# Kernel tuning notes

Hardware: AMD Instinct MI355X
Metric: run time of the kernel (lower is better)

## Reference

```python
import jax, jax.numpy as jnp
import numpy as np

B, EMB, H, G, F, CH, O, OC, KT = 4096, 256, 256, 8, 96, 16, 5, 10, 5
BN_EPS = 1e-3


def _grouped_linear(x, w):
    # x: [B, I], w: [G, I//G, O//G] -> [B, O]
    b = x.shape[0]
    g, ig, og = w.shape
    xg = x.reshape(b, g, ig)
    return jnp.einsum('bgi,gio->bgo', xg, w).reshape(b, g * og)


def _gru_cell(x, h, k, rk, bias):
    # keras GRUCell, reset_after=True; gate order z, r, h; bias: [2, 3H]
    xs = x @ k + bias[0]
    hs = h @ rk + bias[1]
    xz, xr, xh = jnp.split(xs, 3, axis=-1)
    hz, hr, hh = jnp.split(hs, 3, axis=-1)
    z = jax.nn.sigmoid(xz + hz)
    r = jax.nn.sigmoid(xr + hr)
    cand = jnp.tanh(xh + r * hh)
    return z * h + (1.0 - z) * cand


def setup_inputs() -> dict:
    key = jax.random.key(0)
    ks = jax.random.split(key, 20)
    w = lambda i, shape: (jax.random.normal(ks[i], shape, dtype=jnp.float32) * 0.05)
    inp = {
        'emb': jax.random.normal(ks[0], (B, EMB), dtype=jnp.float32),
        'c0': jax.random.normal(ks[1], (B, 1, F, CH), dtype=jnp.float32),
        'df_dec_state': jax.random.normal(ks[2], (B, 2 * H), dtype=jnp.float32),
        'df_convp_buf': jax.random.normal(ks[3], (B, KT - 1, F, CH), dtype=jnp.float32),
        'w_in': w(4, (G, EMB // G, H // G)),
        'gru_k0': w(5, (H, 3 * H)),
        'gru_rk0': w(6, (H, 3 * H)),
        'gru_b0': w(7, (2, 3 * H)),
        'gru_k1': w(8, (H, 3 * H)),
        'gru_rk1': w(9, (H, 3 * H)),
        'gru_b1': w(10, (2, 3 * H)),
        'w_out': w(11, (G, H // G, (F * OC) // G)),
        'fc_a_w': w(12, (H, 1)),
        'fc_a_b': jnp.zeros((1,), dtype=jnp.float32),
        'conv_w': w(13, (KT, 1, CH // 2, OC)),  # grouped conv, groups=gcd(16,10)=2
        'pw_w': w(14, (OC, OC)),                # 1x1 pointwise, no bias
        'bn_gamma': jnp.ones((OC,), dtype=jnp.float32),
        'bn_beta': jnp.zeros((OC,), dtype=jnp.float32),
        'bn_mean': jnp.zeros((OC,), dtype=jnp.float32),
        'bn_var': jnp.ones((OC,), dtype=jnp.float32),
    }
    return inp


def reference(emb, c0, df_dec_state, df_convp_buf,
              w_in, gru_k0, gru_rk0, gru_b0, gru_k1, gru_rk1, gru_b1,
              w_out, fc_a_w, fc_a_b, conv_w, pw_w,
              bn_gamma, bn_beta, bn_mean, bn_var):
    b = emb.shape[0]
    # SqueezedGRUStep: grouped linear in-proj + ReLU
    x_in = jax.nn.relu(_grouped_linear(emb, w_in))  # [B, H]
    h0 = df_dec_state[:, :H]
    h1 = df_dec_state[:, H:]
    out0 = _gru_cell(x_in, h0, gru_k0, gru_rk0, gru_b0)
    out1 = _gru_cell(out0, h1, gru_k1, gru_rk1, gru_b1)
    new_state = jnp.concatenate([out0, out1], axis=-1)  # [B, 2H]
    c = out1 + x_in  # gru_skip = identity

    # causal conv step: concat buffer + current frame -> [B, KT, F, CH]
    x = jnp.concatenate([df_convp_buf, c0], axis=1)
    new_buf = x[:, 1:, :, :]
    # grouped conv (groups=2), kernel (KT,1), valid over the KT frames -> last frame
    xg = x.reshape(b, KT, F, 2, CH // 2)                 # [B,T,F,g,i]
    wg = conv_w.reshape(KT, CH // 2, 2, OC // 2)         # [T,i,g,o]
    y = jnp.einsum('btfgi,tigo->bfgo', xg, wg).reshape(b, F, OC)
    # separable pointwise 1x1 conv
    y = y @ pw_w
    # batch norm (inference) + relu
    inv = jax.lax.rsqrt(bn_var + BN_EPS)
    y = (y - bn_mean) * inv * bn_gamma + bn_beta
    c0_out = jax.nn.relu(y)                              # [B, F, OC]

    alpha = jax.nn.sigmoid(emb @ jnp.zeros_like(fc_a_w) + c @ fc_a_w + fc_a_b)  # [B,1]
    c_out = jnp.tanh(_grouped_linear(c, w_out)).reshape(b, F, OC)
    c_out = c_out + c0_out
    # DfOutputReshapeMF: [B,1,F,O*2] -> [B,O,1,F,2]
    coefs = c_out.reshape(b, 1, F, O, 2).transpose(0, 3, 1, 2, 4)
    return (coefs, alpha, new_state, new_buf)
```

## Files before the change

kernel.cpp:

```cpp
#include <hip/hip_runtime.h>

typedef unsigned short u16;
typedef __attribute__((ext_vector_type(8))) u16 u16x8;
typedef __attribute__((ext_vector_type(8))) __bf16 bf16x8;
typedef __attribute__((ext_vector_type(4))) float f32x4;

#define ALPHA_OFF   3932160
#define NST_OFF     3936256
#define NBUF_OFF    6033408

__device__ __forceinline__ u16 f2bf(float f) {
  unsigned u = __builtin_bit_cast(unsigned, f);
  u += 0x7fffu + ((u >> 16) & 1u);
  return (u16)(u >> 16);
}
__device__ __forceinline__ float bf2f(u16 v) {
  return __builtin_bit_cast(float, (unsigned)v << 16);
}
__device__ __forceinline__ float fsig(float x) { return 1.f / (1.f + __expf(-x)); }
__device__ __forceinline__ float ftanh(float x) {
  x = fminf(15.f, fmaxf(-15.f, x));
  float e = __expf(2.f * x);
  return (e - 1.f) / (e + 1.f);
}
__device__ __forceinline__ f32x4 mfma16(u16x8 a, u16x8 b, f32x4 c) {
  return __builtin_amdgcn_mfma_f32_16x16x32_bf16(
      __builtin_bit_cast(bf16x8, a), __builtin_bit_cast(bf16x8, b), c, 0, 0, 0);
}
__device__ __forceinline__ void gload16(const void* g, void* l) {
  __builtin_amdgcn_global_load_lds(
      (const __attribute__((address_space(1))) void*)g,
      (__attribute__((address_space(3))) void*)l, 16, 0, 0);
}

__global__ __launch_bounds__(256) void prep_all_kernel(
    const float* __restrict__ emb, const float* __restrict__ dec,
    const float* __restrict__ w_in,
    const float* __restrict__ gk0, const float* __restrict__ grk0,
    const float* __restrict__ gk1, const float* __restrict__ grk1,
    const float* __restrict__ w_out,
    u16* __restrict__ A0, u16* __restrict__ A1, u16* __restrict__ W2,
    u16* __restrict__ W3) {
  int bi = blockIdx.x, tid = threadIdx.x;
  if (bi < 192) {
    __shared__ u16 tl[64][65];
    int nb = bi % 12, kb = (bi / 12) % 8, L = bi / 96;
    const float* src = (kb < 4) ? (L ? gk1 : gk0) : (L ? grk1 : grk0);
    int kbase = (kb & 3) * 64;
    u16* dst = W2 + (size_t)L * 768 * 512;
    int c = tid & 63, r4 = tid >> 6;
    for (int rr = 0; rr < 64; rr += 4) {
      int k = kbase + rr + r4, n = nb * 64 + c;
      tl[rr + r4][c] = f2bf(src[(size_t)k * 768 + n]);
    }
    __syncthreads();
    for (int rr = 0; rr < 64; rr += 4) {
      int n = nb * 64 + rr + r4, k = kb * 64 + c;
      dst[(size_t)n * 512 + k] = tl[c][rr + r4];
    }
  } else if (bi < 200) {
    int g = bi - 192;
    for (int i = tid; i < 4096; i += 256) {
      int col = i >> 5, k = i & 31;
      float v = (col < 120) ? w_out[(size_t)g * 3840 + k * 120 + col] : 0.f;
      W3[(size_t)g * 4096 + i] = f2bf(v);
    }
  } else {
    __shared__ float el[4][256];
    int rowBase = (bi - 200) * 4;
    {
      int r = tid >> 6, c4 = tid & 63;
      *(float4*)&el[r][c4 * 4] = ((const float4*)emb)[(size_t)(rowBase + r) * 64 + c4];
    }
    int g = tid >> 5, o = tid & 31;
    float wr[32];
#pragma unroll
    for (int i = 0; i < 32; ++i) wr[i] = w_in[g * 1024 + i * 32 + o];
    __syncthreads();
#pragma unroll
    for (int r = 0; r < 4; ++r) {
      float acc = 0.f;
#pragma unroll
      for (int i = 0; i < 32; ++i) acc += el[r][g * 32 + i] * wr[i];
      A0[(size_t)(rowBase + r) * 512 + tid] = f2bf(fmaxf(acc, 0.f));
    }
    const float4* d4 = (const float4*)dec;
#pragma unroll
    for (int j = 0; j < 2; ++j) {
      int idx = tid + j * 256;
      int r = idx >> 7, c4 = idx & 127;
      float4 v = d4[(size_t)(rowBase + r) * 128 + c4];
      ushort4 q;
      q.x = f2bf(v.x); q.y = f2bf(v.y); q.z = f2bf(v.z); q.w = f2bf(v.w);
      u16* dst = (c4 < 64) ? A0 + (size_t)(rowBase + r) * 512 + 256 + c4 * 4
                           : A1 + (size_t)(rowBase + r) * 512 + 256 + (c4 - 64) * 4;
      *(ushort4*)dst = q;
    }
  }
}

template <int LAYER>
__global__ __launch_bounds__(256) void gru_kernel(
    const u16* __restrict__ Ain,
    const u16* __restrict__ W2,
    const float* __restrict__ dec,
    const float* __restrict__ bias,
    float* __restrict__ nst,
    u16* __restrict__ a1out,
    const u16* __restrict__ xbf,
    u16* __restrict__ c_bf) {
  __shared__ __align__(16) u16 lsA[2][32][32];
  __shared__ __align__(16) u16 lsB[2][3][64][32];
  int tid = threadIdx.x, lane = tid & 63, wave = tid >> 6;
  int m0 = lane & 15, quad = lane >> 4;
  int rowBase = blockIdx.x * 32, jz = blockIdx.y * 64, cw = wave * 16;
  f32x4 acc[4][2];
#pragma unroll
  for (int gi = 0; gi < 4; ++gi)
#pragma unroll
    for (int rb = 0; rb < 2; ++rb) acc[gi][rb] = (f32x4){0.f, 0.f, 0.f, 0.f};

  int rS = tid >> 2, qS = tid & 3;
  auto stage = [&](int buf, int k0) {
    if (tid < 128)
      gload16(Ain + (size_t)(rowBase + rS) * 512 + k0 + qS * 8,
              &lsA[buf][rS][qS * 8]);
#pragma unroll
    for (int g = 0; g < 3; ++g)
      gload16(W2 + (size_t)(g * 256 + jz + rS) * 512 + k0 + qS * 8,
              &lsB[buf][g][rS][qS * 8]);
  };

  stage(0, 0);
  for (int step = 0; step < 16; ++step) {
    __syncthreads();
    if (step < 15) stage((step & 1) ^ 1, (step + 1) * 32);
    int cur = step & 1;
    u16x8 av[2], bv[3];
#pragma unroll
    for (int rb = 0; rb < 2; ++rb)
      av[rb] = *(const u16x8*)&lsA[cur][rb * 16 + m0][quad * 8];
#pragma unroll
    for (int g = 0; g < 3; ++g)
      bv[g] = *(const u16x8*)&lsB[cur][g][cw + m0][quad * 8];
#pragma unroll
    for (int rb = 0; rb < 2; ++rb) {
      acc[0][rb] = mfma16(av[rb], bv[0], acc[0][rb]);
      acc[1][rb] = mfma16(av[rb], bv[1], acc[1][rb]);
    }
    if (step < 8) {
#pragma unroll
      for (int rb = 0; rb < 2; ++rb) acc[2][rb] = mfma16(av[rb], bv[2], acc[2][rb]);
    } else {
#pragma unroll
      for (int rb = 0; rb < 2; ++rb) acc[3][rb] = mfma16(av[rb], bv[2], acc[3][rb]);
    }
  }

  int col = jz + cw + m0;
  float bz = bias[col] + bias[768 + col];
  float br = bias[256 + col] + bias[1024 + col];
  float bxh = bias[512 + col];
  float bhh = bias[1280 + col];
  const int hoff = LAYER ? 256 : 0;
#pragma unroll
  for (int rb = 0; rb < 2; ++rb) {
#pragma unroll
    for (int i = 0; i < 4; ++i) {
      int row = rowBase + rb * 16 + quad * 4 + i;
      float h = dec[(size_t)row * 512 + hoff + col];
      float z = fsig(acc[0][rb][i] + bz);
      float r = fsig(acc[1][rb][i] + br);
      float cand = ftanh(acc[2][rb][i] + bxh + r * (acc[3][rb][i] + bhh));
      float o = z * h + (1.f - z) * cand;
      nst[(size_t)row * 512 + hoff + col] = o;
      if (LAYER == 0) {
        a1out[(size_t)row * 512 + col] = f2bf(o);
      } else {
        float c = o + bf2f(xbf[(size_t)row * 512 + col]);
        c_bf[(size_t)row * 256 + col] = f2bf(c);
      }
    }
  }
}

__global__ __launch_bounds__(256) void wout_kernel(
    const u16* __restrict__ c_bf, const u16* __restrict__ W3,
    float* __restrict__ outc) {
  __shared__ __align__(16) u16 lsA[64][32];
  __shared__ __align__(16) u16 lsB[128][32];
  int tid = threadIdx.x, lane = tid & 63, wave = tid >> 6;
  int m0 = lane & 15, quad = lane >> 4;
  int rowBase = blockIdx.x * 64, g = blockIdx.y;
  {
    int r = tid >> 2, q = tid & 3;
    gload16(c_bf + (size_t)(rowBase + r) * 256 + g * 32 + q * 8, &lsA[r][q * 8]);
    gload16(W3 + (size_t)g * 4096 + (size_t)r * 32 + q * 8, &lsB[r][q * 8]);
    gload16(W3 + (size_t)g * 4096 + (size_t)(64 + r) * 32 + q * 8, &lsB[64 + r][q * 8]);
  }
  __syncthreads();
  int cw = wave * 32;
  f32x4 acc[4][2];
#pragma unroll
  for (int rb = 0; rb < 4; ++rb)
#pragma unroll
    for (int cb = 0; cb < 2; ++cb) acc[rb][cb] = (f32x4){0.f, 0.f, 0.f, 0.f};
  u16x8 bv[2];
#pragma unroll
  for (int cb = 0; cb < 2; ++cb)
    bv[cb] = *(const u16x8*)&lsB[cw + cb * 16 + m0][quad * 8];
#pragma unroll
  for (int rb = 0; rb < 4; ++rb) {
    u16x8 av = *(const u16x8*)&lsA[rb * 16 + m0][quad * 8];
#pragma unroll
    for (int cb = 0; cb < 2; ++cb) acc[rb][cb] = mfma16(av, bv[cb], acc[rb][cb]);
  }
#pragma unroll
  for (int cb = 0; cb < 2; ++cb) {
    int cg = cw + cb * 16 + m0;
    if (cg < 120) {
      int e0 = g * 120 + cg;
      int ff = e0 / 10, p = e0 % 10;
      int fin = (p >> 1) * 192 + ff * 2 + (p & 1);
#pragma unroll
      for (int rb = 0; rb < 4; ++rb)
#pragma unroll
        for (int i = 0; i < 4; ++i)
          outc[(size_t)(rowBase + rb * 16 + quad * 4 + i) * 960 + fin] =
              ftanh(acc[rb][cb][i]);
    }
  }
}

__global__ __launch_bounds__(384) void head_kernel(
    const float* __restrict__ convp, const float* __restrict__ c0,
    const u16* __restrict__ c_bf,
    const float* __restrict__ conv_w, const float* __restrict__ pw_w,
    const float* __restrict__ bng, const float* __restrict__ bnb,
    const float* __restrict__ bnm, const float* __restrict__ bnv,
    const float* __restrict__ fca_w, const float* __restrict__ fca_b,
    float* __restrict__ outp) {
  __shared__ __align__(16) float cw2[640];
  __shared__ float pws[100];
  __shared__ float bsc[10], bsh[10];
  __shared__ float ybuf[2][96][11];
  __shared__ float ared[6];
  int tid = threadIdx.x, lane = tid & 63, wave = tid >> 6;
  int row = tid >= 192, t = tid - row * 192;
  int brow = blockIdx.x * 2 + row;
  int f = t >> 1, half = t & 1;
  const float4* cp4 = (const float4*)convp;
  const float4* c04 = (const float4*)c0;
  float4* nb4 = (float4*)(outp + NBUF_OFF);

  size_t sbase = (size_t)brow * 1536 + f * 4 + half * 2;
  size_t cbase = (size_t)brow * 384 + f * 4 + half * 2;
  float4 xa0 = cp4[sbase];         float4 xb0 = cp4[sbase + 1];
  float4 xa1 = cp4[sbase + 384];   float4 xb1 = cp4[sbase + 385];
  float4 xa2 = cp4[sbase + 768];   float4 xb2 = cp4[sbase + 769];
  float4 xa3 = cp4[sbase + 1152];  float4 xb3 = cp4[sbase + 1153];
  float4 xa4 = c04[cbase];         float4 xb4 = c04[cbase + 1];
  float tmp[5];
#pragma unroll
  for (int k = 0; k < 5; ++k)
    tmp[k] = outp[(size_t)brow * 960 + t + k * 192];
  float ap = bf2f(c_bf[(size_t)brow * 256 + t]) * fca_w[t];
  if (t < 64) ap += bf2f(c_bf[(size_t)brow * 256 + 192 + t]) * fca_w[192 + t];

  for (int i = tid; i < 400; i += 384) {
    int tt = i / 80, rr = (i % 80) / 10, h = (i % 10) / 5, j = i % 5;
    cw2[((tt * 8 + rr) * 2 + h) * 8 + j] = conv_w[i];
  }
  if (tid < 100) pws[tid] = pw_w[tid];
  if (tid < 10) {
    float s = bng[tid] * rsqrtf(bnv[tid] + 1e-3f);
    bsc[tid] = s;
    bsh[tid] = bnb[tid] - bnm[tid] * s;
  }
  nb4[sbase] = xa1;         nb4[sbase + 1] = xb1;
  nb4[sbase + 384] = xa2;   nb4[sbase + 385] = xb2;
  nb4[sbase + 768] = xa3;   nb4[sbase + 769] = xb3;
  nb4[sbase + 1152] = xa4;  nb4[sbase + 1153] = xb4;
#pragma unroll
  for (int off = 32; off > 0; off >>= 1) ap += __shfl_down(ap, off, 64);
  if (lane == 0) ared[wave] = ap;
  __syncthreads();
  float a5[5] = {0.f, 0.f, 0.f, 0.f, 0.f};
#define CI(XF, T, I)                                                        \
  {                                                                         \
    const float* wp = &cw2[(((T) * 8 + (I)) * 2 + half) * 8];               \
    float4 w03 = *(const float4*)wp;                                        \
    float w4 = wp[4];                                                       \
    a5[0] += (XF) * w03.x; a5[1] += (XF) * w03.y; a5[2] += (XF) * w03.z;    \
    a5[3] += (XF) * w03.w; a5[4] += (XF) * w4;                              \
  }
#define CTAP(VA, VB, T)                                                     \
  CI(VA.x, T, 0) CI(VA.y, T, 1) CI(VA.z, T, 2) CI(VA.w, T, 3)               \
  CI(VB.x, T, 4) CI(VB.y, T, 5) CI(VB.z, T, 6) CI(VB.w, T, 7)
  CTAP(xa0, xb0, 0)
  CTAP(xa1, xb1, 1)
  CTAP(xa2, xb2, 2)
  CTAP(xa3, xb3, 3)
  CTAP(xa4, xb4, 4)
#undef CTAP
#undef CI
#pragma unroll
  for (int j = 0; j < 5; ++j) ybuf[row][f][half * 5 + j] = a5[j];
  __syncthreads();
  if (t == 0)
    outp[ALPHA_OFF + brow] =
        fsig(ared[row * 3] + ared[row * 3 + 1] + ared[row * 3 + 2] + fca_b[0]);
  float vals[5];
#pragma unroll
  for (int k = 0; k < 5; ++k) {
    int p = k * 2 + half;
    float y2 = 0.f;
#pragma unroll
    for (int j = 0; j < 10; ++j) y2 += ybuf[row][f][j] * pws[j * 10 + p];
    vals[k] = fmaxf(y2 * bsc[p] + bsh[p], 0.f) + tmp[k];
  }
#pragma unroll
  for (int k = 0; k < 5; ++k)
    outp[(size_t)brow * 960 + t + k * 192] = vals[k];
}

extern "C" void kernel_launch(void* const* d_in, const int* in_sizes, int n_in,
                              void* d_out, int out_size, void* d_ws, size_t ws_size,
                              hipStream_t stream) {
  const float* emb    = (const float*)d_in[0];
  const float* c0     = (const float*)d_in[1];
  const float* dec    = (const float*)d_in[2];
  const float* convp  = (const float*)d_in[3];
  const float* w_in   = (const float*)d_in[4];
  const float* gk0    = (const float*)d_in[5];
  const float* grk0   = (const float*)d_in[6];
  const float* gb0    = (const float*)d_in[7];
  const float* gk1    = (const float*)d_in[8];
  const float* grk1   = (const float*)d_in[9];
  const float* gb1    = (const float*)d_in[10];
  const float* w_out  = (const float*)d_in[11];
  const float* fca_w  = (const float*)d_in[12];
  const float* fca_b  = (const float*)d_in[13];
  const float* conv_w = (const float*)d_in[14];
  const float* pw_w   = (const float*)d_in[15];
  const float* bng    = (const float*)d_in[16];
  const float* bnb    = (const float*)d_in[17];
  const float* bnm    = (const float*)d_in[18];
  const float* bnv    = (const float*)d_in[19];
  float* out = (float*)d_out;
  char* ws = (char*)d_ws;
  u16* A0   = (u16*)(ws + 0);
  u16* A1   = (u16*)(ws + 4194304);
  u16* c_bf = (u16*)(ws + 8388608);
  u16* W2   = (u16*)(ws + 10485760);
  u16* W3   = (u16*)(ws + 12058624);

  prep_all_kernel<<<dim3(1224), 256, 0, stream>>>(emb, dec, w_in,
                                                  gk0, grk0, gk1, grk1, w_out,
                                                  A0, A1, W2, W3);
  gru_kernel<0><<<dim3(128, 4), 256, 0, stream>>>(A0, W2, dec, gb0,
                                                  out + NST_OFF, A1, nullptr, nullptr);
  gru_kernel<1><<<dim3(128, 4), 256, 0, stream>>>(A1, W2 + 768 * 512, dec, gb1,
                                                  out + NST_OFF, nullptr, A0, c_bf);
  wout_kernel<<<dim3(64, 8), 256, 0, stream>>>(c_bf, W3, out);
  head_kernel<<<dim3(2048), 384, 0, stream>>>(convp, c0, c_bf, conv_w, pw_w,
                                              bng, bnb, bnm, bnv, fca_w, fca_b, out);
}
```

Before: 307.0 us.

## Fold conv head into GRU layer-0 launch and alpha into wout kernel

Removes the separate head kernel. Its causal conv, pointwise, BN and buffer-shift work now runs in extra blocks appended to the layer-0 GRU grid, one batch row per block, which lets it overlap with the GEMM blocks. The alpha dot product moves into the g==0 blocks of the wout kernel, and wout now adds tanh output onto the conv result already in the output buffer. This drops one launch and the head's second pass over the output, at the cost of a read-modify-write in wout and 64 idle lanes in each conv block.

Result: no change. 308.8 us (+0.6%).

```diff
diff --git a/kernel.cpp b/kernel.cpp
--- a/kernel.cpp
+++ b/kernel.cpp
@@ -108,12 +108,98 @@
     float* __restrict__ nst,
     u16* __restrict__ a1out,
     const u16* __restrict__ xbf,
-    u16* __restrict__ c_bf) {
-  __shared__ __align__(16) u16 lsA[2][32][32];
-  __shared__ __align__(16) u16 lsB[2][3][64][32];
-  int tid = threadIdx.x, lane = tid & 63, wave = tid >> 6;
+    u16* __restrict__ c_bf,
+    const float* __restrict__ convp, const float* __restrict__ c0f,
+    const float* __restrict__ conv_w, const float* __restrict__ pw_w,
+    const float* __restrict__ bng, const float* __restrict__ bnb,
+    const float* __restrict__ bnm, const float* __restrict__ bnv,
+    float* __restrict__ outp) {
+  __shared__ __align__(16) char smem[28672];
+  int bi = blockIdx.x, tid = threadIdx.x;
+
+  if (LAYER == 0 && bi >= 512) {
+    int b = bi - 512;
+    float* cw2 = (float*)smem;
+    float* pws = (float*)(smem + 2560);
+    float* bscp = (float*)(smem + 2960);
+    float* bshp = (float*)(smem + 3000);
+    float (*ybuf)[11] = (float (*)[11])(smem + 3040);
+    int t = tid, f = t >> 1, half = t & 1;
+    bool act = t < 192;
+    const float4* cp4 = (const float4*)convp;
+    const float4* c04 = (const float4*)c0f;
+    float4* nb4 = (float4*)(outp + NBUF_OFF);
+    size_t sbase = (size_t)b * 1536 + f * 4 + half * 2;
+    size_t cbase = (size_t)b * 384 + f * 4 + half * 2;
+    float4 xa0 = {0,0,0,0}, xb0 = {0,0,0,0}, xa1 = {0,0,0,0}, xb1 = {0,0,0,0};
+    float4 xa2 = {0,0,0,0}, xb2 = {0,0,0,0}, xa3 = {0,0,0,0}, xb3 = {0,0,0,0};
+    float4 xa4 = {0,0,0,0}, xb4 = {0,0,0,0};
+    if (act) {
+      xa0 = cp4[sbase];         xb0 = cp4[sbase + 1];
+      xa1 = cp4[sbase + 384];   xb1 = cp4[sbase + 385];
+      xa2 = cp4[sbase + 768];   xb2 = cp4[sbase + 769];
+      xa3 = cp4[sbase + 1152];  xb3 = cp4[sbase + 1153];
+      xa4 = c04[cbase];         xb4 = c04[cbase + 1];
+    }
+    for (int i = tid; i < 400; i += 256) {
+      int tt = i / 80, rr = (i % 80) / 10, h = (i % 10) / 5, j = i % 5;
+      cw2[((tt * 8 + rr) * 2 + h) * 8 + j] = conv_w[i];
+    }
+    if (tid < 100) pws[tid] = pw_w[tid];
+    if (tid < 10) {
+      float s = bng[tid] * rsqrtf(bnv[tid] + 1e-3f);
+      bscp[tid] = s;
+      bshp[tid] = bnb[tid] - bnm[tid] * s;
+    }
+    if (act) {
+      nb4[sbase] = xa1;         nb4[sbase + 1] = xb1;
+      nb4[sbase + 384] = xa2;   nb4[sbase + 385] = xb2;
+      nb4[sbase + 768] = xa3;   nb4[sbase + 769] = xb3;
+      nb4[sbase + 1152] = xa4;  nb4[sbase + 1153] = xb4;
+    }
+    __syncthreads();
+    if (act) {
+      float a5[5] = {0.f, 0.f, 0.f, 0.f, 0.f};
+#define CI(XF, T, I)                                                        \
+  {                                                                         \
+    const float* wp = &cw2[(((T) * 8 + (I)) * 2 + half) * 8];               \
+    float4 w03 = *(const float4*)wp;                                        \
+    float w4 = wp[4];                                                       \
+    a5[0] += (XF) * w03.x; a5[1] += (XF) * w03.y; a5[2] += (XF) * w03.z;    \
+    a5[3] += (XF) * w03.w; a5[4] += (XF) * w4;                              \
+  }
+#define CTAP(VA, VB, T)                                                     \
+  CI(VA.x, T, 0) CI(VA.y, T, 1) CI(VA.z, T, 2) CI(VA.w, T, 3)               \
+  CI(VB.x, T, 4) CI(VB.y, T, 5) CI(VB.z, T, 6) CI(VB.w, T, 7)
+      CTAP(xa0, xb0, 0)
+      CTAP(xa1, xb1, 1)
+      CTAP(xa2, xb2, 2)
+      CTAP(xa3, xb3, 3)
+      CTAP(xa4, xb4, 4)
+#undef CTAP
+#undef CI
+#pragma unroll
+      for (int j = 0; j < 5; ++j) ybuf[f][half * 5 + j] = a5[j];
+    }
+    __syncthreads();
+    if (act) {
+#pragma unroll
+      for (int k = 0; k < 5; ++k) {
+        int p = k * 2 + half;
+        float y2 = 0.f;
+#pragma unroll
+        for (int j = 0; j < 10; ++j) y2 += ybuf[f][j] * pws[j * 10 + p];
+        outp[(size_t)b * 960 + t + k * 192] = fmaxf(y2 * bscp[p] + bshp[p], 0.f);
+      }
+    }
+    return;
+  }
+
+  auto lsA = (u16 (*)[32][32])smem;
+  auto lsB = (u16 (*)[3][64][32])(smem + 4096);
+  int lane = tid & 63, wave = tid >> 6;
   int m0 = lane & 15, quad = lane >> 4;
-  int rowBase = blockIdx.x * 32, jz = blockIdx.y * 64, cw = wave * 16;
+  int rowBase = (bi >> 2) * 32, jz = (bi & 3) * 64, cw = wave * 16;
   f32x4 acc[4][2];
 #pragma unroll
   for (int gi = 0; gi < 4; ++gi)
@@ -186,6 +272,7 @@
 
 __global__ __launch_bounds__(256) void wout_kernel(
     const u16* __restrict__ c_bf, const u16* __restrict__ W3,
+    const float* __restrict__ fca_w, const float* __restrict__ fca_b,
     float* __restrict__ outc) {
   __shared__ __align__(16) u16 lsA[64][32];
   __shared__ __align__(16) u16 lsB[128][32];
@@ -198,6 +285,21 @@
     gload16(W3 + (size_t)g * 4096 + (size_t)r * 32 + q * 8, &lsB[r][q * 8]);
     gload16(W3 + (size_t)g * 4096 + (size_t)(64 + r) * 32 + q * 8, &lsB[64 + r][q * 8]);
   }
+  if (g == 0) {
+    int r = rowBase + (tid >> 2), q = tid & 3;
+    const u16* crow = c_bf + (size_t)r * 256 + q * 64;
+    const float* fw = fca_w + q * 64;
+    float s = 0.f;
+#pragma unroll
+    for (int i8 = 0; i8 < 8; ++i8) {
+      u16x8 cc = *(const u16x8*)(crow + i8 * 8);
+#pragma unroll
+      for (int j = 0; j < 8; ++j) s += bf2f(cc[j]) * fw[i8 * 8 + j];
+    }
+    s += __shfl_xor(s, 1, 64);
+    s += __shfl_xor(s, 2, 64);
+    if (q == 0) outc[ALPHA_OFF + r] = fsig(s + fca_b[0]);
+  }
   __syncthreads();
   int cw = wave * 32;
   f32x4 acc[4][2];
@@ -225,103 +327,12 @@
 #pragma unroll
       for (int rb = 0; rb < 4; ++rb)
 #pragma unroll
-        for (int i = 0; i < 4; ++i)
-          outc[(size_t)(rowBase + rb * 16 + quad * 4 + i) * 960 + fin] =
-              ftanh(acc[rb][cb][i]);
-    }
-  }
-}
-
-__global__ __launch_bounds__(384) void head_kernel(
-    const float* __restrict__ convp, const float* __restrict__ c0,
-    const u16* __restrict__ c_bf,
-    const float* __restrict__ conv_w, const float* __restrict__ pw_w,
-    const float* __restrict__ bng, const float* __restrict__ bnb,
-    const float* __restrict__ bnm, const float* __restrict__ bnv,
-    const float* __restrict__ fca_w, const float* __restrict__ fca_b,
-    float* __restrict__ outp) {
-  __shared__ __align__(16) float cw2[640];
-  __shared__ float pws[100];
-  __shared__ float bsc[10], bsh[10];
-  __shared__ float ybuf[2][96][11];
-  __shared__ float ared[6];
-  int tid = threadIdx.x, lane = tid & 63, wave = tid >> 6;
-  int row = tid >= 192, t = tid - row * 192;
-  int brow = blockIdx.x * 2 + row;
-  int f = t >> 1, half = t & 1;
-  const float4* cp4 = (const float4*)convp;
-  const float4* c04 = (const float4*)c0;
-  float4* nb4 = (float4*)(outp + NBUF_OFF);
-
-  size_t sbase = (size_t)brow * 1536 + f * 4 + half * 2;
-  size_t cbase = (size_t)brow * 384 + f * 4 + half * 2;
-  float4 xa0 = cp4[sbase];         float4 xb0 = cp4[sbase + 1];
-  float4 xa1 = cp4[sbase + 384];   float4 xb1 = cp4[sbase + 385];
-  float4 xa2 = cp4[sbase + 768];   float4 xb2 = cp4[sbase + 769];
-  float4 xa3 = cp4[sbase + 1152];  float4 xb3 = cp4[sbase + 1153];
-  float4 xa4 = c04[cbase];         float4 xb4 = c04[cbase + 1];
-  float tmp[5];
-#pragma unroll
-  for (int k = 0; k < 5; ++k)
-    tmp[k] = outp[(size_t)brow * 960 + t + k * 192];
-  float ap = bf2f(c_bf[(size_t)brow * 256 + t]) * fca_w[t];
-  if (t < 64) ap += bf2f(c_bf[(size_t)brow * 256 + 192 + t]) * fca_w[192 + t];
-
-  for (int i = tid; i < 400; i += 384) {
-    int tt = i / 80, rr = (i % 80) / 10, h = (i % 10) / 5, j = i % 5;
-    cw2[((tt * 8 + rr) * 2 + h) * 8 + j] = conv_w[i];
-  }
-  if (tid < 100) pws[tid] = pw_w[tid];
-  if (tid < 10) {
-    float s = bng[tid] * rsqrtf(bnv[tid] + 1e-3f);
-    bsc[tid] = s;
-    bsh[tid] = bnb[tid] - bnm[tid] * s;
-  }
-  nb4[sbase] = xa1;         nb4[sbase + 1] = xb1;
-  nb4[sbase + 384] = xa2;   nb4[sbase + 385] = xb2;
-  nb4[sbase + 768] = xa3;   nb4[sbase + 769] = xb3;
-  nb4[sbase + 1152] = xa4;  nb4[sbase + 1153] = xb4;
-#pragma unroll
-  for (int off = 32; off > 0; off >>= 1) ap += __shfl_down(ap, off, 64);
-  if (lane == 0) ared[wave] = ap;
-  __syncthreads();
-  float a5[5] = {0.f, 0.f, 0.f, 0.f, 0.f};
-#define CI(XF, T, I)                                                        \
-  {                                                                         \
-    const float* wp = &cw2[(((T) * 8 + (I)) * 2 + half) * 8];               \
-    float4 w03 = *(const float4*)wp;                                        \
-    float w4 = wp[4];                                                       \
-    a5[0] += (XF) * w03.x; a5[1] += (XF) * w03.y; a5[2] += (XF) * w03.z;    \
-    a5[3] += (XF) * w03.w; a5[4] += (XF) * w4;                              \
-  }
-#define CTAP(VA, VB, T)                                                     \
-  CI(VA.x, T, 0) CI(VA.y, T, 1) CI(VA.z, T, 2) CI(VA.w, T, 3)               \
-  CI(VB.x, T, 4) CI(VB.y, T, 5) CI(VB.z, T, 6) CI(VB.w, T, 7)
-  CTAP(xa0, xb0, 0)
-  CTAP(xa1, xb1, 1)
-  CTAP(xa2, xb2, 2)
-  CTAP(xa3, xb3, 3)
-  CTAP(xa4, xb4, 4)
-#undef CTAP
-#undef CI
-#pragma unroll
-  for (int j = 0; j < 5; ++j) ybuf[row][f][half * 5 + j] = a5[j];
-  __syncthreads();
-  if (t == 0)
-    outp[ALPHA_OFF + brow] =
-        fsig(ared[row * 3] + ared[row * 3 + 1] + ared[row * 3 + 2] + fca_b[0]);
-  float vals[5];
-#pragma unroll
-  for (int k = 0; k < 5; ++k) {
-    int p = k * 2 + half;
-    float y2 = 0.f;
-#pragma unroll
-    for (int j = 0; j < 10; ++j) y2 += ybuf[row][f][j] * pws[j * 10 + p];
-    vals[k] = fmaxf(y2 * bsc[p] + bsh[p], 0.f) + tmp[k];
-  }
-#pragma unroll
-  for (int k = 0; k < 5; ++k)
-    outp[(size_t)brow * 960 + t + k * 192] = vals[k];
+        for (int i = 0; i < 4; ++i) {
+          size_t addr = (size_t)(rowBase + rb * 16 + quad * 4 + i) * 960 + fin;
+          outc[addr] = outc[addr] + ftanh(acc[rb][cb][i]);
+        }
+    }
+  }
 }
 
 extern "C" void kernel_launch(void* const* d_in, const int* in_sizes, int n_in,
@@ -358,11 +369,13 @@
   prep_all_kernel<<<dim3(1224), 256, 0, stream>>>(emb, dec, w_in,
                                                   gk0, grk0, gk1, grk1, w_out,
                                                   A0, A1, W2, W3);
-  gru_kernel<0><<<dim3(128, 4), 256, 0, stream>>>(A0, W2, dec, gb0,
-                                                  out + NST_OFF, A1, nullptr, nullptr);
-  gru_kernel<1><<<dim3(128, 4), 256, 0, stream>>>(A1, W2 + 768 * 512, dec, gb1,
-                                                  out + NST_OFF, nullptr, A0, c_bf);
-  wout_kernel<<<dim3(64, 8), 256, 0, stream>>>(c_bf, W3, out);
-  head_kernel<<<dim3(2048), 384, 0, stream>>>(convp, c0, c_bf, conv_w, pw_w,
-                                              bng, bnb, bnm, bnv, fca_w, fca_b, out);
-}
+  gru_kernel<0><<<dim3(4608), 256, 0, stream>>>(A0, W2, dec, gb0,
+                                                out + NST_OFF, A1, nullptr, nullptr,
+                                                convp, c0, conv_w, pw_w,
+                                                bng, bnb, bnm, bnv, out);
+  gru_kernel<1><<<dim3(512), 256, 0, stream>>>(A1, W2 + 768 * 512, dec, gb1,
+                                               out + NST_OFF, nullptr, A0, c_bf,
+                                               convp, c0, conv_w, pw_w,
+                                               bng, bnb, bnm, bnv, out);
+  wout_kernel<<<dim3(64, 8), 256, 0, stream>>>(c_bf, W3, fca_w, fca_b, out);
+}
```
